# Performance work log

Measured on AMD Instinct MI355X. Metric: run time of the kernel, lower is better.

## Reference

```python
import jax, jax.numpy as jnp
import numpy as np

B, S, UNITS = 32, 4096, 512

def setup_inputs() -> dict:
    key = jax.random.key(0)
    ks = jax.random.split(key, 5)
    scale = 1.0 / np.sqrt(UNITS)
    return {
        "s_prev": jax.random.normal(ks[0], (B, UNITS), dtype=jnp.float32),
        "hidden_states": jax.random.normal(ks[1], (B, S, UNITS), dtype=jnp.float32),
        "Ww": jax.random.normal(ks[2], (UNITS, UNITS), dtype=jnp.float32) * scale,
        "Wb": jnp.zeros((UNITS,), dtype=jnp.float32),
        "Uw": jax.random.normal(ks[3], (UNITS, UNITS), dtype=jnp.float32) * scale,
        "Ub": jnp.zeros((UNITS,), dtype=jnp.float32),
        "Vw": jax.random.normal(ks[4], (UNITS, 1), dtype=jnp.float32) * scale,
        "Vb": jnp.zeros((1,), dtype=jnp.float32),
    }

def reference(s_prev, hidden_states, Ww, Wb, Uw, Ub, Vw, Vb):
    # W(s_prev): [B, 1, U] so it broadcasts over seq axis
    W_s = (s_prev @ Ww + Wb)[:, None, :]
    # U(hidden_states): [B, S, U]
    U_h = jnp.einsum('bsu,uv->bsv', hidden_states, Uw) + Ub
    score = jnp.tanh(W_s + U_h)                      # [B, S, U]
    logits = jnp.einsum('bsu,uo->bso', score, Vw) + Vb  # [B, S, 1]
    weights = jax.nn.softmax(logits, axis=1)         # softmax over seq axis
    context = jnp.sum(weights * hidden_states, axis=1)  # [B, U]
    return (context, weights)
```

## Files before the change

kernel.cpp:

```cpp
#include <hip/hip_runtime.h>
#include <hip/hip_bf16.h>

#define UNITS 512
#define SEQ   4096
#define BATCH 32

typedef __attribute__((ext_vector_type(8))) __bf16 bf16x8;
typedef __attribute__((ext_vector_type(4))) float  f32x4;

__device__ __forceinline__ int swzB(int l) { return l ^ (((l >> 6) & 7) << 4); }

#define MFMA(A, B, C) __builtin_amdgcn_mfma_f32_16x16x32_bf16(A, B, C, 0, 0, 0)
#define GLL(SRC, DST) __builtin_amdgcn_global_load_lds( \
    (const __attribute__((address_space(1))) void*)(SRC), \
    (__attribute__((address_space(3))) void*)(DST), 16, 0, 0)

__global__ void k_bprep(const float* __restrict__ Uw, __bf16* __restrict__ UwTt) {
    const int kstep = blockIdx.x;
    const int q     = blockIdx.y;
    const int t     = threadIdx.x;
    const int nl    = t & 127;
    const int h     = t >> 7;
    const int n     = q * 128 + nl;
    const int k0    = kstep * 32 + h * 16;
    bf16x8 o0, o1;
#pragma unroll
    for (int j = 0; j < 8; j++) {
        o0[j] = (__bf16)Uw[(size_t)(k0 + j) * UNITS + n];
        o1[j] = (__bf16)Uw[(size_t)(k0 + 8 + j) * UNITS + n];
    }
    char* base = (char*)UwTt + (size_t)(kstep * 4 + q) * 8192;
    *(bf16x8*)(base + swzB(nl * 64 + h * 32))      = o0;
    *(bf16x8*)(base + swzB(nl * 64 + h * 32 + 16)) = o1;
}

__global__ void k_wsrow(const float* __restrict__ s_prev, const float* __restrict__ Ww,
                        const float* __restrict__ Wb, const float* __restrict__ Ub,
                        float* __restrict__ ws_Ws) {
    __shared__ float sp[UNITS];
    int b = blockIdx.x, t = threadIdx.x;
    sp[t] = s_prev[b * UNITS + t];
    sp[t + 256] = s_prev[b * UNITS + t + 256];
    __syncthreads();
    float a0 = Wb[t] + Ub[t];
    float a1 = Wb[t + 256] + Ub[t + 256];
#pragma unroll 8
    for (int u = 0; u < UNITS; u++) {
        float s = sp[u];
        a0 += s * Ww[u * UNITS + t];
        a1 += s * Ww[u * UNITS + t + 256];
    }
    ws_Ws[b * UNITS + t] = a0;
    ws_Ws[b * UNITS + t + 256] = a1;
}

#define BM 128
#define BN 128
#define BK 32
#define NSTEP (UNITS / BK)

__launch_bounds__(256, 4)
__global__ void k_logits(const float* __restrict__ hidden, const __bf16* __restrict__ UwTt,
                         const float* __restrict__ wsu, const float* __restrict__ Vw,
                         float* __restrict__ lpart) {
    __shared__ __bf16 Ab[2][BM * BK];
    __shared__ __bf16 Bb[2][BN * BK];
    __shared__ float  lred[BM][2];

    const int t = threadIdx.x;
    const int lane = t & 63, wv = t >> 6;
    const int wm = wv >> 1, wn = wv & 1;
    const int l15 = lane & 15, l4 = lane >> 4;

    const int id = blockIdx.x;
    const int gx = (id >> 3) & 3;
    const int mt = ((id >> 5) << 3) | (id & 7);
    const int m0 = mt * BM;
    const int b  = m0 >> 12;

    f32x4 acc[4][4];
#pragma unroll
    for (int i = 0; i < 4; i++)
#pragma unroll
        for (int j = 0; j < 4; j++) acc[i][j] = (f32x4){0.f, 0.f, 0.f, 0.f};

    const int sr = t >> 1;
    const int sh = t & 1;
    const float* aRow = hidden + (size_t)(m0 + sr) * UNITS + sh * 16;
    const int aw0 = swzB(sr * 64 + sh * 32);
    const int aw1 = swzB(sr * 64 + sh * 32 + 16);

    int aoffR[4], boffR[4];
#pragma unroll
    for (int f = 0; f < 4; f++) {
        aoffR[f] = swzB((wm * 64 + f * 16 + l15) * 64 + l4 * 16);
        boffR[f] = swzB((wn * 64 + f * 16 + l15) * 64 + l4 * 16);
    }

    const char* bglBase = (const char*)UwTt + (size_t)gx * 8192 + wv * 2048 + lane * 16;

    {
        float4 v0 = *(const float4*)(aRow);
        float4 v1 = *(const float4*)(aRow + 4);
        float4 v2 = *(const float4*)(aRow + 8);
        float4 v3 = *(const float4*)(aRow + 12);
        GLL(bglBase,        (char*)Bb[0] + wv * 2048);
        GLL(bglBase + 1024, (char*)Bb[0] + wv * 2048 + 1024);
        bf16x8 o0, o1;
        o0[0]=(__bf16)v0.x; o0[1]=(__bf16)v0.y; o0[2]=(__bf16)v0.z; o0[3]=(__bf16)v0.w;
        o0[4]=(__bf16)v1.x; o0[5]=(__bf16)v1.y; o0[6]=(__bf16)v1.z; o0[7]=(__bf16)v1.w;
        o1[0]=(__bf16)v2.x; o1[1]=(__bf16)v2.y; o1[2]=(__bf16)v2.z; o1[3]=(__bf16)v2.w;
        o1[4]=(__bf16)v3.x; o1[5]=(__bf16)v3.y; o1[6]=(__bf16)v3.z; o1[7]=(__bf16)v3.w;
        *(bf16x8*)((char*)Ab[0] + aw0) = o0;
        *(bf16x8*)((char*)Ab[0] + aw1) = o1;
    }

#pragma unroll 2
    for (int s = 0; s < NSTEP; ++s) {
        const int cur = s & 1;
        __syncthreads();

        float4 v0, v1, v2, v3;
        if (s + 1 < NSTEP) {
            v0 = *(const float4*)(aRow + (s + 1) * BK);
            v1 = *(const float4*)(aRow + (s + 1) * BK + 4);
            v2 = *(const float4*)(aRow + (s + 1) * BK + 8);
            v3 = *(const float4*)(aRow + (s + 1) * BK + 12);
            GLL(bglBase + (size_t)((s + 1) * 4) * 8192,
                (char*)Bb[cur ^ 1] + wv * 2048);
            GLL(bglBase + (size_t)((s + 1) * 4) * 8192 + 1024,
                (char*)Bb[cur ^ 1] + wv * 2048 + 1024);
        }

        bf16x8 a[4], bq[4];
#pragma unroll
        for (int fi = 0; fi < 4; fi++)
            a[fi] = *(const bf16x8*)((const char*)Ab[cur] + aoffR[fi]);
#pragma unroll
        for (int fj = 0; fj < 4; fj++)
            bq[fj] = *(const bf16x8*)((const char*)Bb[cur] + boffR[fj]);
#pragma unroll
        for (int fi = 0; fi < 4; fi++)
#pragma unroll
            for (int fj = 0; fj < 4; fj++)
                acc[fi][fj] = MFMA(a[fi], bq[fj], acc[fi][fj]);

        if (s + 1 < NSTEP) {
            bf16x8 o0, o1;
            o0[0]=(__bf16)v0.x; o0[1]=(__bf16)v0.y; o0[2]=(__bf16)v0.z; o0[3]=(__bf16)v0.w;
            o0[4]=(__bf16)v1.x; o0[5]=(__bf16)v1.y; o0[6]=(__bf16)v1.z; o0[7]=(__bf16)v1.w;
            o1[0]=(__bf16)v2.x; o1[1]=(__bf16)v2.y; o1[2]=(__bf16)v2.z; o1[3]=(__bf16)v2.w;
            o1[4]=(__bf16)v3.x; o1[5]=(__bf16)v3.y; o1[6]=(__bf16)v3.z; o1[7]=(__bf16)v3.w;
            *(bf16x8*)((char*)Ab[cur ^ 1] + aw0) = o0;
            *(bf16x8*)((char*)Ab[cur ^ 1] + aw1) = o1;
        }
    }

    float wsub[4], vww[4];
#pragma unroll
    for (int fj = 0; fj < 4; fj++) {
        int n = gx * BN + wn * 64 + fj * 16 + l15;
        wsub[fj] = wsu[b * UNITS + n];
        vww[fj]  = Vw[n];
    }
#pragma unroll
    for (int fi = 0; fi < 4; fi++) {
#pragma unroll
        for (int r = 0; r < 4; r++) {
            float p = 0.f;
#pragma unroll
            for (int fj = 0; fj < 4; fj++) {
                float x = acc[fi][fj][r] + wsub[fj];
                float e = __expf(2.f * x);
                p += vww[fj] * (1.f - 2.f / (e + 1.f));
            }
#pragma unroll
            for (int off = 1; off < 16; off <<= 1) p += __shfl_xor(p, off);
            if (l15 == 0) lred[wm * 64 + fi * 16 + l4 * 4 + r][wn] = p;
        }
    }
    __syncthreads();
    if (t < BM) {
        lpart[(size_t)(m0 + t) * 4 + gx] = lred[t][0] + lred[t][1];
    }
}

__global__ void k_softmax(const float* __restrict__ lpart, float* __restrict__ wout) {
    __shared__ float ebuf[SEQ];
    __shared__ float red[8];
    int b = blockIdx.x, t = threadIdx.x;
    int lane = t & 63, wv = t >> 6;
    float m = -1e30f;
#pragma unroll
    for (int i = 0; i < 16; i++) {
        int s = t + i * 256;
        size_t idx = ((size_t)b * SEQ + s) * 4;
        float l = (lpart[idx] + lpart[idx + 1]) + (lpart[idx + 2] + lpart[idx + 3]);
        ebuf[s] = l;
        m = fmaxf(m, l);
    }
#pragma unroll
    for (int off = 32; off >= 1; off >>= 1) m = fmaxf(m, __shfl_xor(m, off));
    if (lane == 0) red[wv] = m;
    __syncthreads();
    m = fmaxf(fmaxf(red[0], red[1]), fmaxf(red[2], red[3]));
    float zs = 0.f;
#pragma unroll
    for (int i = 0; i < 16; i++) {
        int s = t + i * 256;
        float e = __expf(ebuf[s] - m);
        ebuf[s] = e;
        zs += e;
    }
#pragma unroll
    for (int off = 32; off >= 1; off >>= 1) zs += __shfl_xor(zs, off);
    __syncthreads();
    if (lane == 0) red[wv] = zs;
    __syncthreads();
    float inv = 1.f / (red[0] + red[1] + red[2] + red[3]);
#pragma unroll
    for (int i = 0; i < 16; i++) {
        int s = t + i * 256;
        wout[(size_t)b * SEQ + s] = ebuf[s] * inv;
    }
}

__global__ void k_ctxpart(const float* __restrict__ hidden, const float* __restrict__ wout,
                          float* __restrict__ part) {
    int b = blockIdx.y, c = blockIdx.x, t = threadIdx.x;
    const float* w = wout + (size_t)b * SEQ + c * 128;
    const float* h = hidden + ((size_t)b * SEQ + c * 128) * UNITS;
    float2 acc = make_float2(0.f, 0.f);
#pragma unroll 4
    for (int s = 0; s < 128; s++) {
        float ww = w[s];
        float2 v = ((const float2*)(h + (size_t)s * UNITS))[t];
        acc.x += ww * v.x;
        acc.y += ww * v.y;
    }
    ((float2*)(part + ((size_t)(b * 32 + c)) * UNITS))[t] = acc;
}

__global__ void k_ctxreduce(const float* __restrict__ part, float* __restrict__ ctx) {
    int b = blockIdx.x, t = threadIdx.x;
    float s = 0.f;
#pragma unroll
    for (int c = 0; c < 32; c++) s += part[((size_t)(b * 32 + c)) * UNITS + t];
    ctx[(size_t)b * UNITS + t] = s;
}

extern "C" void kernel_launch(void* const* d_in, const int* in_sizes, int n_in,
                              void* d_out, int out_size, void* d_ws, size_t ws_size,
                              hipStream_t stream) {
    const float* s_prev = (const float*)d_in[0];
    const float* hidden = (const float*)d_in[1];
    const float* Ww     = (const float*)d_in[2];
    const float* Wb     = (const float*)d_in[3];
    const float* Uw     = (const float*)d_in[4];
    const float* Ub     = (const float*)d_in[5];
    const float* Vw     = (const float*)d_in[6];

    float* out  = (float*)d_out;
    float* ctx  = out;
    float* wout = out + BATCH * UNITS;

    float* wsf   = (float*)d_ws;
    float* ws_Ws = wsf;
    float* ws_lp = ws_Ws + BATCH * UNITS;
    float* ws_cp = ws_lp + (size_t)BATCH * SEQ * 4;
    __bf16* UwTt = (__bf16*)(ws_cp + (size_t)BATCH * 32 * UNITS);

    k_bprep<<<dim3(16, 4), dim3(256), 0, stream>>>(Uw, UwTt);
    k_wsrow<<<dim3(32), dim3(256), 0, stream>>>(s_prev, Ww, Wb, Ub, ws_Ws);
    k_logits<<<dim3(4096), dim3(256), 0, stream>>>(hidden, UwTt, ws_Ws, Vw, ws_lp);
    k_softmax<<<dim3(32), dim3(256), 0, stream>>>(ws_lp, wout);
    k_ctxpart<<<dim3(32, 32), dim3(256), 0, stream>>>(hidden, wout, ws_cp);
    k_ctxreduce<<<dim3(32), dim3(512), 0, stream>>>(ws_cp, ctx);
}
```

Measured before the change: 224.4 us.

## Load A operand directly into MFMA registers, bypassing LDS, with manual vmcnt pipeline

The hidden-state (A) tile no longer goes through shared memory. Each lane loads the fp32 rows it needs for its MFMA fragments straight from global memory, packs them to bf16 in registers, and prefetches two k-steps ahead. Synchronisation is now done by hand with explicit s_waitcnt counts and raw s_barrier, and the k-loop is fully unrolled. This removes the LDS write/read round trip and the associated barrier traffic for A, but each wave now reloads rows that other waves also read. Register pressure also rises, so launch bounds drop to 3 blocks per CU.

```diff
diff --git a/kernel.cpp b/kernel.cpp
--- a/kernel.cpp
+++ b/kernel.cpp
@@ -14,6 +14,10 @@
 #define GLL(SRC, DST) __builtin_amdgcn_global_load_lds( \
     (const __attribute__((address_space(1))) void*)(SRC), \
     (__attribute__((address_space(3))) void*)(DST), 16, 0, 0)
+#define PK8(X, Y) ({ bf16x8 _o; \
+    _o[0]=(__bf16)(X).x; _o[1]=(__bf16)(X).y; _o[2]=(__bf16)(X).z; _o[3]=(__bf16)(X).w; \
+    _o[4]=(__bf16)(Y).x; _o[5]=(__bf16)(Y).y; _o[6]=(__bf16)(Y).z; _o[7]=(__bf16)(Y).w; _o; })
+#define FENCE() asm volatile("" ::: "memory")
 
 __global__ void k_bprep(const float* __restrict__ Uw, __bf16* __restrict__ UwTt) {
     const int kstep = blockIdx.x;
@@ -59,11 +63,10 @@
 #define BK 32
 #define NSTEP (UNITS / BK)
 
-__launch_bounds__(256, 4)
+__launch_bounds__(256, 3)
 __global__ void k_logits(const float* __restrict__ hidden, const __bf16* __restrict__ UwTt,
                          const float* __restrict__ wsu, const float* __restrict__ Vw,
                          float* __restrict__ lpart) {
-    __shared__ __bf16 Ab[2][BM * BK];
     __shared__ __bf16 Bb[2][BN * BK];
     __shared__ float  lred[BM][2];
 
@@ -84,75 +87,77 @@
 #pragma unroll
         for (int j = 0; j < 4; j++) acc[i][j] = (f32x4){0.f, 0.f, 0.f, 0.f};
 
-    const int sr = t >> 1;
-    const int sh = t & 1;
-    const float* aRow = hidden + (size_t)(m0 + sr) * UNITS + sh * 16;
-    const int aw0 = swzB(sr * 64 + sh * 32);
-    const int aw1 = swzB(sr * 64 + sh * 32 + 16);
-
-    int aoffR[4], boffR[4];
+    const float* aF[4];
+#pragma unroll
+    for (int f = 0; f < 4; f++)
+        aF[f] = hidden + (size_t)(m0 + wm * 64 + f * 16 + l15) * UNITS + l4 * 8;
+
+    int boffR[4];
+#pragma unroll
+    for (int f = 0; f < 4; f++)
+        boffR[f] = swzB((wn * 64 + f * 16 + l15) * 64 + l4 * 16);
+
+    const char* bglBase = (const char*)UwTt + (size_t)gx * 8192 + wv * 2048 + lane * 16;
+
+    float4 afl[2][8];
+    bf16x8 apk[4];
+
+    GLL(bglBase,        (char*)Bb[0] + wv * 2048);
+    GLL(bglBase + 1024, (char*)Bb[0] + wv * 2048 + 1024);
+    FENCE();
 #pragma unroll
     for (int f = 0; f < 4; f++) {
-        aoffR[f] = swzB((wm * 64 + f * 16 + l15) * 64 + l4 * 16);
-        boffR[f] = swzB((wn * 64 + f * 16 + l15) * 64 + l4 * 16);
-    }
-
-    const char* bglBase = (const char*)UwTt + (size_t)gx * 8192 + wv * 2048 + lane * 16;
-
-    {
-        float4 v0 = *(const float4*)(aRow);
-        float4 v1 = *(const float4*)(aRow + 4);
-        float4 v2 = *(const float4*)(aRow + 8);
-        float4 v3 = *(const float4*)(aRow + 12);
-        GLL(bglBase,        (char*)Bb[0] + wv * 2048);
-        GLL(bglBase + 1024, (char*)Bb[0] + wv * 2048 + 1024);
-        bf16x8 o0, o1;
-        o0[0]=(__bf16)v0.x; o0[1]=(__bf16)v0.y; o0[2]=(__bf16)v0.z; o0[3]=(__bf16)v0.w;
-        o0[4]=(__bf16)v1.x; o0[5]=(__bf16)v1.y; o0[6]=(__bf16)v1.z; o0[7]=(__bf16)v1.w;
-        o1[0]=(__bf16)v2.x; o1[1]=(__bf16)v2.y; o1[2]=(__bf16)v2.z; o1[3]=(__bf16)v2.w;
-        o1[4]=(__bf16)v3.x; o1[5]=(__bf16)v3.y; o1[6]=(__bf16)v3.z; o1[7]=(__bf16)v3.w;
-        *(bf16x8*)((char*)Ab[0] + aw0) = o0;
-        *(bf16x8*)((char*)Ab[0] + aw1) = o1;
-    }
-
-#pragma unroll 2
+        afl[0][2 * f]     = *(const float4*)(aF[f]);
+        afl[0][2 * f + 1] = *(const float4*)(aF[f] + 4);
+    }
+    FENCE();
+#pragma unroll
+    for (int f = 0; f < 4; f++) {
+        afl[1][2 * f]     = *(const float4*)(aF[f] + BK);
+        afl[1][2 * f + 1] = *(const float4*)(aF[f] + BK + 4);
+    }
+    asm volatile("s_waitcnt vmcnt(16)" ::: "memory");
+    __builtin_amdgcn_s_barrier();
+#pragma unroll
+    for (int f = 0; f < 4; f++)
+        apk[f] = PK8(afl[0][2 * f], afl[0][2 * f + 1]);
+
+#pragma unroll
     for (int s = 0; s < NSTEP; ++s) {
         const int cur = s & 1;
-        __syncthreads();
-
-        float4 v0, v1, v2, v3;
-        if (s + 1 < NSTEP) {
-            v0 = *(const float4*)(aRow + (s + 1) * BK);
-            v1 = *(const float4*)(aRow + (s + 1) * BK + 4);
-            v2 = *(const float4*)(aRow + (s + 1) * BK + 8);
-            v3 = *(const float4*)(aRow + (s + 1) * BK + 12);
-            GLL(bglBase + (size_t)((s + 1) * 4) * 8192,
-                (char*)Bb[cur ^ 1] + wv * 2048);
-            GLL(bglBase + (size_t)((s + 1) * 4) * 8192 + 1024,
-                (char*)Bb[cur ^ 1] + wv * 2048 + 1024);
-        }
-
-        bf16x8 a[4], bq[4];
-#pragma unroll
-        for (int fi = 0; fi < 4; fi++)
-            a[fi] = *(const bf16x8*)((const char*)Ab[cur] + aoffR[fi]);
+        bf16x8 bq[4];
 #pragma unroll
         for (int fj = 0; fj < 4; fj++)
             bq[fj] = *(const bf16x8*)((const char*)Bb[cur] + boffR[fj]);
+        if (s + 1 < NSTEP) {
+            const char* bs = bglBase + (size_t)(s + 1) * 32768;
+            GLL(bs,        (char*)Bb[cur ^ 1] + wv * 2048);
+            GLL(bs + 1024, (char*)Bb[cur ^ 1] + wv * 2048 + 1024);
+        }
+        FENCE();
+        if (s + 2 < NSTEP) {
+#pragma unroll
+            for (int f = 0; f < 4; f++) {
+                afl[cur][2 * f]     = *(const float4*)(aF[f] + (s + 2) * BK);
+                afl[cur][2 * f + 1] = *(const float4*)(aF[f] + (s + 2) * BK + 4);
+            }
+        }
+        asm volatile("s_waitcnt lgkmcnt(0)" ::: "memory");
+        __builtin_amdgcn_sched_barrier(0);
 #pragma unroll
         for (int fi = 0; fi < 4; fi++)
 #pragma unroll
             for (int fj = 0; fj < 4; fj++)
-                acc[fi][fj] = MFMA(a[fi], bq[fj], acc[fi][fj]);
-
+                acc[fi][fj] = MFMA(apk[fi], bq[fj], acc[fi][fj]);
         if (s + 1 < NSTEP) {
-            bf16x8 o0, o1;
-            o0[0]=(__bf16)v0.x; o0[1]=(__bf16)v0.y; o0[2]=(__bf16)v0.z; o0[3]=(__bf16)v0.w;
-            o0[4]=(__bf16)v1.x; o0[5]=(__bf16)v1.y; o0[6]=(__bf16)v1.z; o0[7]=(__bf16)v1.w;
-            o1[0]=(__bf16)v2.x; o1[1]=(__bf16)v2.y; o1[2]=(__bf16)v2.z; o1[3]=(__bf16)v2.w;
-            o1[4]=(__bf16)v3.x; o1[5]=(__bf16)v3.y; o1[6]=(__bf16)v3.z; o1[7]=(__bf16)v3.w;
-            *(bf16x8*)((char*)Ab[cur ^ 1] + aw0) = o0;
-            *(bf16x8*)((char*)Ab[cur ^ 1] + aw1) = o1;
+            if (s + 2 < NSTEP) asm volatile("s_waitcnt vmcnt(10)" ::: "memory");
+            else               asm volatile("s_waitcnt vmcnt(2)"  ::: "memory");
+#pragma unroll
+            for (int f = 0; f < 4; f++)
+                apk[f] = PK8(afl[cur ^ 1][2 * f], afl[cur ^ 1][2 * f + 1]);
+            if (s + 2 < NSTEP) asm volatile("s_waitcnt vmcnt(8)" ::: "memory");
+            else               asm volatile("s_waitcnt vmcnt(0)" ::: "memory");
+            __builtin_amdgcn_s_barrier();
         }
     }
 
```

After: 441.8 us. +96.9%, slower.
